# Performance work log

Hardware: AMD Instinct MI355X
Metric: run time of the kernel (lower is better)

## Reference

```python
import jax, jax.numpy as jnp
import numpy as np

B, T, D, H = 64, 2048, 256, 5


def setup_inputs() -> dict:
    key = jax.random.key(0)
    ks = jax.random.split(key, 4)
    return {
        "x_temp": jax.random.normal(ks[0], (B, T, D), dtype=jnp.float32),
        "x_fea": jax.random.normal(ks[1], (B, T), dtype=jnp.float32),
        "mask": jnp.ones((B, T), dtype=bool),
        "W_temp": jax.random.normal(ks[2], (D, H), dtype=jnp.float32) * 0.05,
        "b_temp": jnp.zeros((H,), dtype=jnp.float32),
        "W_fea": jax.random.normal(ks[3], (1, H), dtype=jnp.float32) * 0.05,
        "b_fea": jnp.zeros((H,), dtype=jnp.float32),
        "b": jnp.zeros((H,), dtype=jnp.float32),
        "uw": jax.random.normal(jax.random.fold_in(key, 7), (H, H), dtype=jnp.float32) * 0.05,
    }


def reference(x_temp, x_fea, mask, W_temp, b_temp, W_fea, b_fea, b, uw):
    # temp: (B,T,H) projection of features
    temp = jnp.einsum("btd,dh->bth", x_temp, W_temp) + b_temp
    # fea: (B,T,H) projection of the scalar per-timestep feature
    fea = x_fea[..., None] * W_fea[0] + b_fea
    hadamard = jnp.tanh(temp) * jnp.tanh(fea)            # (B,T,H)
    intermed = jnp.sum(hadamard @ uw + b, axis=-1)       # (B,T)
    weights = jax.nn.softmax(intermed, axis=-1)          # (B,T)
    m = mask.astype(jnp.float32)
    weights = weights * m
    weights = weights / jnp.sum(weights, axis=-1, keepdims=True)
    return jnp.sum(x_temp * weights[..., None], axis=1)  # (B,D)
```

## Files before the change

kernel.cpp:

```cpp
#include <hip/hip_runtime.h>
#include <hip/hip_bf16.h>
#include <math.h>

constexpr int BB    = 64;
constexpr int TT    = 2048;
constexpr int DD    = 256;
constexpr int HH    = 5;
constexpr int SEG   = 16;
constexpr int TSEG  = TT / SEG;
constexpr int TC    = 32;
constexpr int STRIDE= 260;

__device__ __forceinline__ float ftanh(float x) {
    float e = __expf(2.0f * x);
    return 1.0f - 2.0f * __builtin_amdgcn_rcpf(e + 1.0f);
}

__global__ __launch_bounds__(256, 4)
void seg_kernel(const float* __restrict__ x_temp,
                const float* __restrict__ x_fea,
                const int* __restrict__ mask,
                const float* __restrict__ W_temp,
                const float* __restrict__ b_temp,
                const float* __restrict__ W_fea,
                const float* __restrict__ b_fea,
                const float* __restrict__ uw,
                float* __restrict__ part)
{
    __shared__ float ldsx[TC * STRIDE];
    __shared__ float ldsi[TC];

    const int tid  = threadIdx.x;
    const int lane = tid & 63;
    const int wave = tid >> 6;
    const int half = lane >> 5;
    const int l32  = lane & 31;
    const int blk  = blockIdx.x;
    const int b    = blk / SEG;
    const int seg  = blk % SEG;
    const int t0   = seg * TSEG;

    const int dbase = l32 * 8;
    float wv[8][HH];
#pragma unroll
    for (int e = 0; e < 8; ++e)
#pragma unroll
        for (int h = 0; h < HH; ++h)
            wv[e][h] = W_temp[(dbase + e) * HH + h];

    float wfea[HH], bfea[HH], btmp[HH], uwr[HH];
#pragma unroll
    for (int h = 0; h < HH; ++h) {
        wfea[h] = W_fea[h];
        bfea[h] = b_fea[h];
        btmp[h] = b_temp[h];
        float s = 0.f;
#pragma unroll
        for (int h2 = 0; h2 < HH; ++h2) s += uw[h * HH + h2];
        uwr[h] = s;
    }

    float m = -INFINITY, l = 0.f, acc = 0.f;
    const size_t rowbase = (size_t)b * TT;

    for (int c = 0; c < TSEG / TC; ++c) {
        const int tbase = t0 + c * TC;

#pragma unroll
        for (int p = 0; p < 4; ++p) {
            const int tl = wave * 8 + p * 2 + half;
            const int t  = tbase + tl;
            const float4* xr = (const float4*)(x_temp + (rowbase + t) * (size_t)DD);
            float4 a0 = xr[l32 * 2 + 0];
            float4 a1 = xr[l32 * 2 + 1];

            float* row = &ldsx[tl * STRIDE + dbase];
            *(float4*)(row)     = a0;
            *(float4*)(row + 4) = a1;

            float ph[HH];
#pragma unroll
            for (int h = 0; h < HH; ++h)
                ph[h] = a0.x * wv[0][h] + a0.y * wv[1][h] + a0.z * wv[2][h] + a0.w * wv[3][h]
                      + a1.x * wv[4][h] + a1.y * wv[5][h] + a1.z * wv[6][h] + a1.w * wv[7][h];

#pragma unroll
            for (int off = 16; off >= 1; off >>= 1)
#pragma unroll
                for (int h = 0; h < HH; ++h)
                    ph[h] += __shfl_xor(ph[h], off);

            const float xf = x_fea[rowbase + t];
            float inter = 0.f;
#pragma unroll
            for (int h = 0; h < HH; ++h) {
                float tt = ftanh(ph[h] + btmp[h]);
                float tf = ftanh(xf * wfea[h] + bfea[h]);
                inter += tt * tf * uwr[h];
            }
            if (l32 == 0) ldsi[tl] = inter;
        }
        __syncthreads();

        float cmax = -INFINITY;
#pragma unroll
        for (int t = 0; t < TC; ++t) cmax = fmaxf(cmax, ldsi[t]);
        const float newm = fmaxf(m, cmax);
        const float sc = __expf(m - newm);
        acc *= sc; l *= sc; m = newm;

        const int* mrow = mask + rowbase + tbase;
#pragma unroll 8
        for (int t = 0; t < TC; ++t) {
            float w = mrow[t] ? __expf(ldsi[t] - m) : 0.f;
            l += w;
            acc = fmaf(w, ldsx[t * STRIDE + tid], acc);
        }
        __syncthreads();
    }

    float* pb = part + (size_t)blk * (DD + 2);
    if (tid == 0) { pb[0] = m; pb[1] = l; }
    pb[2 + tid] = acc;
}

__global__ void combine_kernel(const float* __restrict__ part, float* __restrict__ out)
{
    const int b = blockIdx.x;
    const int d = threadIdx.x;
    float M = -INFINITY;
    for (int s = 0; s < SEG; ++s)
        M = fmaxf(M, part[(size_t)(b * SEG + s) * (DD + 2)]);
    float denom = 0.f, num = 0.f;
    for (int s = 0; s < SEG; ++s) {
        const float* p = part + (size_t)(b * SEG + s) * (DD + 2);
        float sc = __expf(p[0] - M);
        denom += sc * p[1];
        num   += sc * p[2 + d];
    }
    out[(size_t)b * DD + d] = num / denom;
}

extern "C" void kernel_launch(void* const* d_in, const int* in_sizes, int n_in,
                              void* d_out, int out_size, void* d_ws, size_t ws_size,
                              hipStream_t stream) {
    const float* x_temp = (const float*)d_in[0];
    const float* x_fea  = (const float*)d_in[1];
    const int*   mask   = (const int*)d_in[2];
    const float* W_temp = (const float*)d_in[3];
    const float* b_temp = (const float*)d_in[4];
    const float* W_fea  = (const float*)d_in[5];
    const float* b_fea  = (const float*)d_in[6];
    const float* uw     = (const float*)d_in[8];

    float* part = (float*)d_ws;
    float* out  = (float*)d_out;

    seg_kernel<<<BB * SEG, 256, 0, stream>>>(x_temp, x_fea, mask, W_temp,
                                             b_temp, W_fea, b_fea, uw, part);
    combine_kernel<<<BB, DD, 0, stream>>>(part, out);
}
```

Before: 221.2 us.

## Split time into 64 segments and keep x tiles in registers

Each batch row is now split into 64 segments of 32 timesteps, so the grid has four times as many blocks. Each block loads its 32 rows of x into registers once, computes the scores, runs a single-pass softmax over the segment, and accumulates directly from registers. The LDS staging of x and the online rescaling loop are gone, and per-row partials are reduced across waves through a small LDS buffer. In exchange, register pressure rises (launch bounds drop to 3 blocks per CU) and the combine kernel has more partials to merge.

New measurement: 222.3 us. About the same (+0.5%).

```diff
diff --git a/kernel.cpp b/kernel.cpp
--- a/kernel.cpp
+++ b/kernel.cpp
@@ -2,21 +2,21 @@
 #include <hip/hip_bf16.h>
 #include <math.h>
 
-constexpr int BB    = 64;
-constexpr int TT    = 2048;
-constexpr int DD    = 256;
-constexpr int HH    = 5;
-constexpr int SEG   = 16;
-constexpr int TSEG  = TT / SEG;
-constexpr int TC    = 32;
-constexpr int STRIDE= 260;
+constexpr int BB   = 64;
+constexpr int TT   = 2048;
+constexpr int DD   = 256;
+constexpr int HH   = 5;
+constexpr int SEG  = 64;
+constexpr int TSEG = TT / SEG;
+constexpr int PSTR = 264;
+constexpr int WSTR = 264;
 
 __device__ __forceinline__ float ftanh(float x) {
     float e = __expf(2.0f * x);
     return 1.0f - 2.0f * __builtin_amdgcn_rcpf(e + 1.0f);
 }
 
-__global__ __launch_bounds__(256, 4)
+__global__ __launch_bounds__(256, 3)
 void seg_kernel(const float* __restrict__ x_temp,
                 const float* __restrict__ x_fea,
                 const int* __restrict__ mask,
@@ -27,20 +27,32 @@
                 const float* __restrict__ uw,
                 float* __restrict__ part)
 {
-    __shared__ float ldsx[TC * STRIDE];
-    __shared__ float ldsi[TC];
+    __shared__ alignas(16) float im[2 * TSEG];
+    __shared__ alignas(16) float ldsw[8 * WSTR];
 
     const int tid  = threadIdx.x;
-    const int lane = tid & 63;
+    const int l    = tid & 63;
     const int wave = tid >> 6;
-    const int half = lane >> 5;
-    const int l32  = lane & 31;
+    const int half = l >> 5;
+    const int l32  = l & 31;
     const int blk  = blockIdx.x;
-    const int b    = blk / SEG;
-    const int seg  = blk % SEG;
+    const int b    = blk >> 6;
+    const int seg  = blk & (SEG - 1);
     const int t0   = seg * TSEG;
+    const size_t rowbase = (size_t)b * TT;
+    const float* xbase = x_temp + (rowbase + t0) * (size_t)DD;
+
+    if (tid < TSEG) im[2 * tid + 1] = mask[rowbase + t0 + tid] ? 1.0f : 0.0f;
 
     const int dbase = l32 * 8;
+    float4 xq[4][2];
+#pragma unroll
+    for (int it = 0; it < 4; ++it) {
+        const float* p = xbase + it * (8 * DD) + wave * (2 * DD) + half * DD + dbase;
+        xq[it][0] = *(const float4*)(p);
+        xq[it][1] = *(const float4*)(p + 4);
+    }
+
     float wv[8][HH];
 #pragma unroll
     for (int e = 0; e < 8; ++e)
@@ -51,92 +63,95 @@
     float wfea[HH], bfea[HH], btmp[HH], uwr[HH];
 #pragma unroll
     for (int h = 0; h < HH; ++h) {
-        wfea[h] = W_fea[h];
-        bfea[h] = b_fea[h];
-        btmp[h] = b_temp[h];
+        wfea[h] = W_fea[h]; bfea[h] = b_fea[h]; btmp[h] = b_temp[h];
         float s = 0.f;
 #pragma unroll
         for (int h2 = 0; h2 < HH; ++h2) s += uw[h * HH + h2];
         uwr[h] = s;
     }
 
-    float m = -INFINITY, l = 0.f, acc = 0.f;
-    const size_t rowbase = (size_t)b * TT;
-
-    for (int c = 0; c < TSEG / TC; ++c) {
-        const int tbase = t0 + c * TC;
-
 #pragma unroll
-        for (int p = 0; p < 4; ++p) {
-            const int tl = wave * 8 + p * 2 + half;
-            const int t  = tbase + tl;
-            const float4* xr = (const float4*)(x_temp + (rowbase + t) * (size_t)DD);
-            float4 a0 = xr[l32 * 2 + 0];
-            float4 a1 = xr[l32 * 2 + 1];
-
-            float* row = &ldsx[tl * STRIDE + dbase];
-            *(float4*)(row)     = a0;
-            *(float4*)(row + 4) = a1;
-
-            float ph[HH];
+    for (int it = 0; it < 4; ++it) {
+        const int r = it * 8 + wave * 2 + half;
+        const float4 a0 = xq[it][0], a1 = xq[it][1];
+        float ph[HH];
+#pragma unroll
+        for (int h = 0; h < HH; ++h)
+            ph[h] = a0.x * wv[0][h] + a0.y * wv[1][h] + a0.z * wv[2][h] + a0.w * wv[3][h]
+                  + a1.x * wv[4][h] + a1.y * wv[5][h] + a1.z * wv[6][h] + a1.w * wv[7][h];
+#pragma unroll
+        for (int off = 16; off >= 1; off >>= 1)
 #pragma unroll
             for (int h = 0; h < HH; ++h)
-                ph[h] = a0.x * wv[0][h] + a0.y * wv[1][h] + a0.z * wv[2][h] + a0.w * wv[3][h]
-                      + a1.x * wv[4][h] + a1.y * wv[5][h] + a1.z * wv[6][h] + a1.w * wv[7][h];
+                ph[h] += __shfl_xor(ph[h], off);
 
+        const float xf = x_fea[rowbase + t0 + r];
+        float inter = 0.f;
 #pragma unroll
-            for (int off = 16; off >= 1; off >>= 1)
+        for (int h = 0; h < HH; ++h)
+            inter += ftanh(ph[h] + btmp[h]) * ftanh(xf * wfea[h] + bfea[h]) * uwr[h];
+        if (l32 == 0) im[2 * r] = inter;
+    }
+    __syncthreads();
+
+    float M = -INFINITY;
 #pragma unroll
-                for (int h = 0; h < HH; ++h)
-                    ph[h] += __shfl_xor(ph[h], off);
-
-            const float xf = x_fea[rowbase + t];
-            float inter = 0.f;
+    for (int k = 0; k < 16; ++k) {
+        float4 v = *(const float4*)(&im[4 * k]);
+        M = fmaxf(M, fmaxf(v.x, v.z));
+    }
+    float lsum = 0.f;
 #pragma unroll
-            for (int h = 0; h < HH; ++h) {
-                float tt = ftanh(ph[h] + btmp[h]);
-                float tf = ftanh(xf * wfea[h] + bfea[h]);
-                inter += tt * tf * uwr[h];
-            }
-            if (l32 == 0) ldsi[tl] = inter;
-        }
-        __syncthreads();
-
-        float cmax = -INFINITY;
-#pragma unroll
-        for (int t = 0; t < TC; ++t) cmax = fmaxf(cmax, ldsi[t]);
-        const float newm = fmaxf(m, cmax);
-        const float sc = __expf(m - newm);
-        acc *= sc; l *= sc; m = newm;
-
-        const int* mrow = mask + rowbase + tbase;
-#pragma unroll 8
-        for (int t = 0; t < TC; ++t) {
-            float w = mrow[t] ? __expf(ldsi[t] - m) : 0.f;
-            l += w;
-            acc = fmaf(w, ldsx[t * STRIDE + tid], acc);
-        }
-        __syncthreads();
+    for (int k = 0; k < 16; ++k) {
+        float4 v = *(const float4*)(&im[4 * k]);
+        lsum += v.y * __expf(v.x - M) + v.w * __expf(v.z - M);
     }
 
-    float* pb = part + (size_t)blk * (DD + 2);
-    if (tid == 0) { pb[0] = m; pb[1] = l; }
-    pb[2 + tid] = acc;
+    float acc8[8] = {0.f, 0.f, 0.f, 0.f, 0.f, 0.f, 0.f, 0.f};
+#pragma unroll
+    for (int it = 0; it < 4; ++it) {
+        const int r = it * 8 + wave * 2 + half;
+        const float w = im[2 * r + 1] * __expf(im[2 * r] - M);
+        const float4 a0 = xq[it][0], a1 = xq[it][1];
+        acc8[0] = fmaf(w, a0.x, acc8[0]); acc8[1] = fmaf(w, a0.y, acc8[1]);
+        acc8[2] = fmaf(w, a0.z, acc8[2]); acc8[3] = fmaf(w, a0.w, acc8[3]);
+        acc8[4] = fmaf(w, a1.x, acc8[4]); acc8[5] = fmaf(w, a1.y, acc8[5]);
+        acc8[6] = fmaf(w, a1.z, acc8[6]); acc8[7] = fmaf(w, a1.w, acc8[7]);
+    }
+
+    const int slot = wave * 2 + half;
+    float* wp = &ldsw[slot * WSTR + dbase];
+    *(float4*)(wp)     = make_float4(acc8[0], acc8[1], acc8[2], acc8[3]);
+    *(float4*)(wp + 4) = make_float4(acc8[4], acc8[5], acc8[6], acc8[7]);
+    __syncthreads();
+
+    float accd = 0.f;
+#pragma unroll
+    for (int s = 0; s < 8; ++s) accd += ldsw[s * WSTR + tid];
+
+    float* pb = part + (size_t)blk * PSTR;
+    if (tid == 0) pb[0] = M;
+    if (tid == 1) pb[1] = lsum;
+    pb[2 + tid] = accd;
 }
 
-__global__ void combine_kernel(const float* __restrict__ part, float* __restrict__ out)
+__global__ __launch_bounds__(256)
+void combine_kernel(const float* __restrict__ part, float* __restrict__ out)
 {
     const int b = blockIdx.x;
     const int d = threadIdx.x;
+    const float* base = part + (size_t)b * SEG * PSTR;
     float M = -INFINITY;
+#pragma unroll 8
     for (int s = 0; s < SEG; ++s)
-        M = fmaxf(M, part[(size_t)(b * SEG + s) * (DD + 2)]);
+        M = fmaxf(M, base[(size_t)s * PSTR]);
     float denom = 0.f, num = 0.f;
+#pragma unroll 4
     for (int s = 0; s < SEG; ++s) {
-        const float* p = part + (size_t)(b * SEG + s) * (DD + 2);
+        const float* p = base + (size_t)s * PSTR;
         float sc = __expf(p[0] - M);
-        denom += sc * p[1];
-        num   += sc * p[2 + d];
+        denom = fmaf(sc, p[1], denom);
+        num   = fmaf(sc, p[2 + d], num);
     }
     out[(size_t)b * DD + d] = num / denom;
 }
```
